# Optimization experiments

Hardware: AMD Instinct MI355X
Metric: run time of the kernel (lower is better)

## Reference

```python
import jax, jax.numpy as jnp
import numpy as np

WINDOW = 9
REG_WEIGHT = 1.0


def _box_filter(x, k):
    """Sum over a k^3 box via three separable 1D ones-convs (== conv3d with ones kernel)."""
    pad = k // 2
    for ax in range(3):  # D, H, W spatial axes
        kshape = [1, 1, 1, 1, 1]
        kshape[2 + ax] = k
        kern = jnp.ones(kshape, x.dtype)
        padding = [(pad, pad) if i == ax else (0, 0) for i in range(3)]
        x = jax.lax.conv_general_dilated(
            x, kern, window_strides=(1, 1, 1), padding=padding,
            dimension_numbers=("NCDHW", "OIDHW", "NCDHW"))
    return x


def _ncc_loss(pred, target, k):
    win_size = jnp.asarray(float(k ** 3), pred.dtype)
    pred_sum = _box_filter(pred, k)
    target_sum = _box_filter(target, k)
    pred_sq_sum = _box_filter(pred * pred, k)
    target_sq_sum = _box_filter(target * target, k)
    pred_target_sum = _box_filter(pred * target, k)
    pred_mean = pred_sum / win_size
    target_mean = target_sum / win_size
    cross = (pred_target_sum - target_mean * pred_sum - pred_mean * target_sum
             + pred_mean * target_mean * win_size)
    pred_var = pred_sq_sum - 2.0 * pred_mean * pred_sum + pred_mean * pred_mean * win_size
    target_var = target_sq_sum - 2.0 * target_mean * target_sum + target_mean * target_mean * win_size
    pred_var = jnp.clip(pred_var, 0.0, None)
    target_var = jnp.clip(target_var, 0.0, None)
    cc = cross * cross / (pred_var * target_var + 0.001)
    cc = jnp.clip(cc, 0.0, 1.0)
    return 1.0 - jnp.mean(cc)


def _gradient_loss(flow):
    dy = jnp.abs(flow[:, :, 1:, :, :] - flow[:, :, :-1, :, :])
    dx = jnp.abs(flow[:, :, :, 1:, :] - flow[:, :, :, :-1, :])
    dz = jnp.abs(flow[:, :, :, :, 1:] - flow[:, :, :, :, :-1])
    return (jnp.mean(dy) + jnp.mean(dx) + jnp.mean(dz)) / 3.0


def setup_inputs() -> dict:
    key = jax.random.key(0)
    k1, k2, k3 = jax.random.split(key, 3)
    B, D, H, W = 2, 160, 160, 160
    moved = jax.random.uniform(k1, (B, 1, D, H, W), dtype=jnp.float32)
    fixed = jax.random.uniform(k2, (B, 1, D, H, W), dtype=jnp.float32)
    flow = jax.random.normal(k3, (B, 3, D, H, W), dtype=jnp.float32)
    return {"moved": moved, "fixed": fixed, "flow": flow}


def reference(moved, fixed, flow):
    sim_loss = _ncc_loss(moved, fixed, WINDOW)
    reg_loss = _gradient_loss(flow)
    total_loss = sim_loss + REG_WEIGHT * reg_loss
    return total_loss
```

## Files before the change

### kernel.cpp

```cpp
#include <hip/hip_runtime.h>

#define DD 160
#define HH 160
#define WW 160
#define VOL (DD * HH * WW)
#define PLANE (HH * WW)
#define NB 2

#define CH 20
#define NDSP (DD / CH)
#define DSBLK (PLANE / 1024)
#define NDSUM (DSBLK * NDSP * NB)

#define GCHD 20
#define GBLK (NB * 3 * (DD / GCHD) * HH * (WW / 4) / 256)

#define HT 16
#define HS (HT + 8)
#define LDWH 168
#define WHBLK ((HH / HT) * DD * NB)

typedef _Float16 h8 __attribute__((ext_vector_type(8)));
typedef _Float16 h4 __attribute__((ext_vector_type(4)));

__global__ __launch_bounds__(256) void stream_pass(const float* __restrict__ mv,
                                                   const float* __restrict__ fx,
                                                   const float* __restrict__ fl,
                                                   _Float16* __restrict__ fields,
                                                   float* __restrict__ pg) {
    const int bx  = blockIdx.x;
    const int tid = threadIdx.x;

    if (bx < NDSUM) {
        const int qt  = bx % DSBLK;
        const int rem = bx / DSBLK;
        const int dsp = rem % NDSP;
        const int b   = rem / NDSP;
        const int hw  = (qt * 256 + tid) * 4;
        const int c0  = dsp * CH;
        const int cend = c0 + CH;

        const float* pm = mv + (size_t)b * VOL + hw;
        const float* pf = fx + (size_t)b * VOL + hw;
        _Float16*    fb = fields + (size_t)b * 5 * VOL + hw;

        float4 s0 = {0,0,0,0}, s1 = {0,0,0,0}, s2 = {0,0,0,0},
               s3 = {0,0,0,0}, s4 = {0,0,0,0};

#define ACC4(m4, f4, sgn)                                              \
        s0.x sgn m4.x; s0.y sgn m4.y; s0.z sgn m4.z; s0.w sgn m4.w;    \
        s1.x sgn f4.x; s1.y sgn f4.y; s1.z sgn f4.z; s1.w sgn f4.w;    \
        s2.x sgn m4.x * m4.x; s2.y sgn m4.y * m4.y;                    \
        s2.z sgn m4.z * m4.z; s2.w sgn m4.w * m4.w;                    \
        s3.x sgn f4.x * f4.x; s3.y sgn f4.y * f4.y;                    \
        s3.z sgn f4.z * f4.z; s3.w sgn f4.w * f4.w;                    \
        s4.x sgn m4.x * f4.x; s4.y sgn m4.y * f4.y;                    \
        s4.z sgn m4.z * f4.z; s4.w sgn m4.w * f4.w;

        {
            int lo = c0 - 4 > 0 ? c0 - 4 : 0;
            int hi = c0 + 4 < DD - 1 ? c0 + 4 : DD - 1;
            for (int dd = lo; dd <= hi; ++dd) {
                float4 m4 = *(const float4*)(pm + (size_t)dd * PLANE);
                float4 f4 = *(const float4*)(pf + (size_t)dd * PLANE);
                ACC4(m4, f4, +=)
            }
        }

        for (int d = c0; d < cend; ++d) {
            _Float16* o = fb + (size_t)d * PLANE;
            h4 t;
            t.x = (_Float16)s0.x; t.y = (_Float16)s0.y; t.z = (_Float16)s0.z; t.w = (_Float16)s0.w;
            *(h4*)(o + 0 * (size_t)VOL) = t;
            t.x = (_Float16)s1.x; t.y = (_Float16)s1.y; t.z = (_Float16)s1.z; t.w = (_Float16)s1.w;
            *(h4*)(o + 1 * (size_t)VOL) = t;
            t.x = (_Float16)s2.x; t.y = (_Float16)s2.y; t.z = (_Float16)s2.z; t.w = (_Float16)s2.w;
            *(h4*)(o + 2 * (size_t)VOL) = t;
            t.x = (_Float16)s3.x; t.y = (_Float16)s3.y; t.z = (_Float16)s3.z; t.w = (_Float16)s3.w;
            *(h4*)(o + 3 * (size_t)VOL) = t;
            t.x = (_Float16)s4.x; t.y = (_Float16)s4.y; t.z = (_Float16)s4.z; t.w = (_Float16)s4.w;
            *(h4*)(o + 4 * (size_t)VOL) = t;

            if (d + 1 < cend) {
                if (d + 5 < DD) {
                    float4 m4 = *(const float4*)(pm + (size_t)(d + 5) * PLANE);
                    float4 f4 = *(const float4*)(pf + (size_t)(d + 5) * PLANE);
                    ACC4(m4, f4, +=)
                }
                if (d - 4 >= 0) {
                    float4 m4 = *(const float4*)(pm + (size_t)(d - 4) * PLANE);
                    float4 f4 = *(const float4*)(pf + (size_t)(d - 4) * PLANE);
                    ACC4(m4, f4, -=)
                }
            }
        }
#undef ACC4
        return;
    }

    const int gid = (bx - NDSUM) * 256 + tid;
    const int w4  = gid % 40;
    int t = gid / 40;
    const int h  = t % HH;  t /= HH;
    const int dc = t % (DD / GCHD); t /= (DD / GCHD);
    const int bc = t;
    const int d0 = dc * GCHD;
    const int w  = w4 * 4;

    const float* base = fl + (size_t)bc * VOL;
    float acc = 0.f;
    float4 v = *(const float4*)(base + ((size_t)d0 * HH + h) * WW + w);
    for (int d = d0; d < d0 + GCHD; ++d) {
        const float* pd = base + ((size_t)d * HH + h) * WW + w;
        float4 vn = v;
        if (d < DD - 1) {
            vn = *(const float4*)(pd + PLANE);
            acc += fabsf(vn.x - v.x) + fabsf(vn.y - v.y) +
                   fabsf(vn.z - v.z) + fabsf(vn.w - v.w);
        }
        if (h < HH - 1) {
            float4 vh = *(const float4*)(pd + WW);
            acc += fabsf(vh.x - v.x) + fabsf(vh.y - v.y) +
                   fabsf(vh.z - v.z) + fabsf(vh.w - v.w);
        }
        acc += fabsf(v.y - v.x) + fabsf(v.z - v.y) + fabsf(v.w - v.z);
        if (w < WW - 4) acc += fabsf(pd[4] - v.w);
        v = vn;
    }

    for (int o = 32; o > 0; o >>= 1) acc += __shfl_down(acc, o, 64);
    __shared__ float red[4];
    int lane = tid & 63, wid = tid >> 6;
    if (lane == 0) red[wid] = acc;
    __syncthreads();
    if (tid == 0) pg[bx - NDSUM] = red[0] + red[1] + red[2] + red[3];
}

__global__ __launch_bounds__(512, 6) void ncc_whcc(const _Float16* __restrict__ fields,
                                                   float* __restrict__ partial) {
    __shared__ _Float16 ws[5][HS][LDWH];
    __shared__ float red[8];

    const int hx  = blockIdx.x;
    const int d   = blockIdx.y;
    const int b   = blockIdx.z;
    const int h0  = hx * HT;
    const int tid = threadIdx.x;

    if (tid < 480) {
        const int r  = tid / 20;
        const int s  = tid - r * 20;
        const int h  = h0 - 4 + r;
        const int w0 = 8 * s;
        const bool rowok = (unsigned)h < (unsigned)HH;

#pragma unroll
        for (int f = 0; f < 5; ++f) {
            float v[16];
#pragma unroll
            for (int i = 0; i < 16; ++i) v[i] = 0.f;
            if (rowok) {
                const _Float16* fr = fields + (size_t)(b * 5 + f) * VOL
                                            + ((size_t)d * HH + h) * WW;
                if (s > 0) {
                    h4 a = *(const h4*)(fr + w0 - 4);
                    v[0] = (float)a.x; v[1] = (float)a.y; v[2] = (float)a.z; v[3] = (float)a.w;
                }
                h4 a1 = *(const h4*)(fr + w0);
                v[4] = (float)a1.x; v[5] = (float)a1.y; v[6] = (float)a1.z; v[7] = (float)a1.w;
                h4 a2 = *(const h4*)(fr + w0 + 4);
                v[8] = (float)a2.x; v[9] = (float)a2.y; v[10] = (float)a2.z; v[11] = (float)a2.w;
                if (s < 19) {
                    h4 a3 = *(const h4*)(fr + w0 + 8);
                    v[12] = (float)a3.x; v[13] = (float)a3.y; v[14] = (float)a3.z; v[15] = (float)a3.w;
                }
            }
            float o[8];
            float sum = 0.f;
#pragma unroll
            for (int i = 0; i < 9; ++i) sum += v[i];
            o[0] = sum;
#pragma unroll
            for (int k = 1; k < 8; ++k) {
                sum += v[k + 8] - v[k - 1];
                o[k] = sum;
            }
            h8 pk;
#pragma unroll
            for (int j = 0; j < 8; ++j) pk[j] = (_Float16)o[j];
            *(h8*)&ws[f][r][w0] = pk;
        }
    }
    __syncthreads();

    float acc = 0.f;
    if (tid < 320) {
        const int ro  = tid / 20;
        const int oct = tid - ro * 20;
        const int w   = 8 * oct;

        float s0[8], s1[8], s2[8], s3[8], s4[8];
#pragma unroll
        for (int j = 0; j < 8; ++j) { s0[j]=0.f; s1[j]=0.f; s2[j]=0.f; s3[j]=0.f; s4[j]=0.f; }
#pragma unroll
        for (int t = 0; t < 9; ++t) {
            h8 v0 = *(const h8*)&ws[0][ro + t][w];
            h8 v1 = *(const h8*)&ws[1][ro + t][w];
            h8 v2 = *(const h8*)&ws[2][ro + t][w];
            h8 v3 = *(const h8*)&ws[3][ro + t][w];
            h8 v4 = *(const h8*)&ws[4][ro + t][w];
#pragma unroll
            for (int j = 0; j < 8; ++j) {
                s0[j] += (float)v0[j]; s1[j] += (float)v1[j];
                s2[j] += (float)v2[j]; s3[j] += (float)v3[j];
                s4[j] += (float)v4[j];
            }
        }
        const float inv_win = 1.0f / 729.0f;
#pragma unroll
        for (int j = 0; j < 8; ++j) {
            float cross = fmaf(-(s0[j] * s1[j]), inv_win, s4[j]);
            float pv = fmaxf(fmaf(-(s0[j] * s0[j]), inv_win, s2[j]), 0.f);
            float tv = fmaxf(fmaf(-(s1[j] * s1[j]), inv_win, s3[j]), 0.f);
            float cc = cross * cross / (pv * tv + 0.001f);
            acc += fminf(fmaxf(cc, 0.f), 1.f);
        }
    }

    for (int o = 32; o > 0; o >>= 1) acc += __shfl_down(acc, o, 64);
    int lane = tid & 63, wid = tid >> 6;
    if (lane == 0) red[wid] = acc;
    __syncthreads();
    if (tid == 0) {
        float r8 = 0.f;
#pragma unroll
        for (int i = 0; i < 8; ++i) r8 += red[i];
        partial[((size_t)b * DD + d) * (HH / HT) + hx] = r8;
    }
}

__global__ __launch_bounds__(256) void finalize(const float* __restrict__ pcc, int ncc,
                                                const float* __restrict__ pg, int ng,
                                                float* __restrict__ out) {
    __shared__ float red[4];
    int lane = threadIdx.x & 63, wid = threadIdx.x >> 6;

    float a = 0.f;
    for (int i = threadIdx.x; i < ncc; i += 256) a += pcc[i];
    for (int o = 32; o > 0; o >>= 1) a += __shfl_down(a, o, 64);
    if (lane == 0) red[wid] = a;
    __syncthreads();
    float asum = red[0] + red[1] + red[2] + red[3];
    __syncthreads();

    float g = 0.f;
    for (int i = threadIdx.x; i < ng; i += 256) g += pg[i];
    for (int o = 32; o > 0; o >>= 1) g += __shfl_down(g, o, 64);
    if (lane == 0) red[wid] = g;
    __syncthreads();
    float gsum = red[0] + red[1] + red[2] + red[3];

    if (threadIdx.x == 0) {
        float sim = 1.0f - asum / 8192000.0f;
        float reg = gsum / 73267200.0f;
        out[0] = sim + reg;
    }
}

extern "C" void kernel_launch(void* const* d_in, const int* in_sizes, int n_in,
                              void* d_out, int out_size, void* d_ws, size_t ws_size,
                              hipStream_t stream) {
    const float* moved  = (const float*)d_in[0];
    const float* fixedp = (const float*)d_in[1];
    const float* flow   = (const float*)d_in[2];
    float* out = (float*)d_out;

    _Float16* fields = (_Float16*)d_ws;
    float* pcc = (float*)(fields + (size_t)NB * 5 * VOL);
    float* pg  = pcc + WHBLK;

    stream_pass<<<NDSUM + GBLK, 256, 0, stream>>>(moved, fixedp, flow, fields, pg);
    ncc_whcc<<<dim3(HH / HT, DD, NB), 512, 0, stream>>>(fields, pcc);
    finalize<<<1, 256, 0, stream>>>(pcc, WHBLK, pg, GBLK, out);
}
```

Measured before the change: 115.4 us.

## Split gradient reduction into separate kernel and batch depth-sum stores in groups

The gradient-loss reduction moves out of the fused stream kernel into its own kernel, launched after the NCC kernel. The D-axis sliding-sum kernel now buffers five consecutive depth slices of all five fields in registers and issues their stores together, grouped by field. The aim is to give the store path more independent writes in flight and to cut branching in the depth-sum kernel. The cost is an extra kernel launch, and the gradient work no longer shares a grid with the depth-sum work, so it cannot fill idle compute units there.

```diff
diff --git a/kernel.cpp b/kernel.cpp
--- a/kernel.cpp
+++ b/kernel.cpp
@@ -7,79 +7,80 @@
 #define PLANE (HH * WW)
 #define NB 2
 
-#define CH 20
-#define NDSP (DD / CH)
+#define DCH 20
+#define NDSP (DD / DCH)
 #define DSBLK (PLANE / 1024)
 #define NDSUM (DSBLK * NDSP * NB)
-
-#define GCHD 20
-#define GBLK (NB * 3 * (DD / GCHD) * HH * (WW / 4) / 256)
+#define BG 5
 
 #define HT 16
 #define HS (HT + 8)
 #define LDWH 168
 #define WHBLK ((HH / HT) * DD * NB)
 
+#define GCHD 20
+#define GBLK (NB * 3 * (DD / GCHD) * HH * (WW / 4) / 256)
+
 typedef _Float16 h8 __attribute__((ext_vector_type(8)));
 typedef _Float16 h4 __attribute__((ext_vector_type(4)));
 
-__global__ __launch_bounds__(256) void stream_pass(const float* __restrict__ mv,
-                                                   const float* __restrict__ fx,
-                                                   const float* __restrict__ fl,
-                                                   _Float16* __restrict__ fields,
-                                                   float* __restrict__ pg) {
+__global__ __launch_bounds__(256) void dsum(const float* __restrict__ mv,
+                                            const float* __restrict__ fx,
+                                            _Float16* __restrict__ fields) {
     const int bx  = blockIdx.x;
     const int tid = threadIdx.x;
 
-    if (bx < NDSUM) {
-        const int qt  = bx % DSBLK;
-        const int rem = bx / DSBLK;
-        const int dsp = rem % NDSP;
-        const int b   = rem / NDSP;
-        const int hw  = (qt * 256 + tid) * 4;
-        const int c0  = dsp * CH;
-        const int cend = c0 + CH;
-
-        const float* pm = mv + (size_t)b * VOL + hw;
-        const float* pf = fx + (size_t)b * VOL + hw;
-        _Float16*    fb = fields + (size_t)b * 5 * VOL + hw;
-
-        float4 s0 = {0,0,0,0}, s1 = {0,0,0,0}, s2 = {0,0,0,0},
-               s3 = {0,0,0,0}, s4 = {0,0,0,0};
+    const int qt  = bx % DSBLK;
+    const int rem = bx / DSBLK;
+    const int dsp = rem % NDSP;
+    const int b   = rem / NDSP;
+    const int hw  = (qt * 256 + tid) * 4;
+    const int c0  = dsp * DCH;
+    const int cend = c0 + DCH;
+
+    const float* pm = mv + (size_t)b * VOL + hw;
+    const float* pf = fx + (size_t)b * VOL + hw;
+    _Float16*    fb = fields + (size_t)b * 5 * VOL + hw;
+
+    float4 s0 = {0,0,0,0}, s1 = {0,0,0,0}, s2 = {0,0,0,0},
+           s3 = {0,0,0,0}, s4 = {0,0,0,0};
 
 #define ACC4(m4, f4, sgn)                                              \
-        s0.x sgn m4.x; s0.y sgn m4.y; s0.z sgn m4.z; s0.w sgn m4.w;    \
-        s1.x sgn f4.x; s1.y sgn f4.y; s1.z sgn f4.z; s1.w sgn f4.w;    \
-        s2.x sgn m4.x * m4.x; s2.y sgn m4.y * m4.y;                    \
-        s2.z sgn m4.z * m4.z; s2.w sgn m4.w * m4.w;                    \
-        s3.x sgn f4.x * f4.x; s3.y sgn f4.y * f4.y;                    \
-        s3.z sgn f4.z * f4.z; s3.w sgn f4.w * f4.w;                    \
-        s4.x sgn m4.x * f4.x; s4.y sgn m4.y * f4.y;                    \
-        s4.z sgn m4.z * f4.z; s4.w sgn m4.w * f4.w;
-
-        {
-            int lo = c0 - 4 > 0 ? c0 - 4 : 0;
-            int hi = c0 + 4 < DD - 1 ? c0 + 4 : DD - 1;
-            for (int dd = lo; dd <= hi; ++dd) {
-                float4 m4 = *(const float4*)(pm + (size_t)dd * PLANE);
-                float4 f4 = *(const float4*)(pf + (size_t)dd * PLANE);
-                ACC4(m4, f4, +=)
-            }
-        }
-
-        for (int d = c0; d < cend; ++d) {
-            _Float16* o = fb + (size_t)d * PLANE;
-            h4 t;
-            t.x = (_Float16)s0.x; t.y = (_Float16)s0.y; t.z = (_Float16)s0.z; t.w = (_Float16)s0.w;
-            *(h4*)(o + 0 * (size_t)VOL) = t;
-            t.x = (_Float16)s1.x; t.y = (_Float16)s1.y; t.z = (_Float16)s1.z; t.w = (_Float16)s1.w;
-            *(h4*)(o + 1 * (size_t)VOL) = t;
-            t.x = (_Float16)s2.x; t.y = (_Float16)s2.y; t.z = (_Float16)s2.z; t.w = (_Float16)s2.w;
-            *(h4*)(o + 2 * (size_t)VOL) = t;
-            t.x = (_Float16)s3.x; t.y = (_Float16)s3.y; t.z = (_Float16)s3.z; t.w = (_Float16)s3.w;
-            *(h4*)(o + 3 * (size_t)VOL) = t;
-            t.x = (_Float16)s4.x; t.y = (_Float16)s4.y; t.z = (_Float16)s4.z; t.w = (_Float16)s4.w;
-            *(h4*)(o + 4 * (size_t)VOL) = t;
+    s0.x sgn m4.x; s0.y sgn m4.y; s0.z sgn m4.z; s0.w sgn m4.w;        \
+    s1.x sgn f4.x; s1.y sgn f4.y; s1.z sgn f4.z; s1.w sgn f4.w;        \
+    s2.x sgn m4.x * m4.x; s2.y sgn m4.y * m4.y;                        \
+    s2.z sgn m4.z * m4.z; s2.w sgn m4.w * m4.w;                        \
+    s3.x sgn f4.x * f4.x; s3.y sgn f4.y * f4.y;                        \
+    s3.z sgn f4.z * f4.z; s3.w sgn f4.w * f4.w;                        \
+    s4.x sgn m4.x * f4.x; s4.y sgn m4.y * f4.y;                        \
+    s4.z sgn m4.z * f4.z; s4.w sgn m4.w * f4.w;
+
+    {
+        int lo = c0 - 4 > 0 ? c0 - 4 : 0;
+        int hi = c0 + 4 < DD - 1 ? c0 + 4 : DD - 1;
+        for (int dd = lo; dd <= hi; ++dd) {
+            float4 m4 = *(const float4*)(pm + (size_t)dd * PLANE);
+            float4 f4 = *(const float4*)(pf + (size_t)dd * PLANE);
+            ACC4(m4, f4, +=)
+        }
+    }
+
+#pragma unroll
+    for (int g = 0; g < DCH / BG; ++g) {
+        h4 buf[BG][5];
+#pragma unroll
+        for (int k = 0; k < BG; ++k) {
+            const int d = c0 + g * BG + k;
+            buf[k][0].x = (_Float16)s0.x; buf[k][0].y = (_Float16)s0.y;
+            buf[k][0].z = (_Float16)s0.z; buf[k][0].w = (_Float16)s0.w;
+            buf[k][1].x = (_Float16)s1.x; buf[k][1].y = (_Float16)s1.y;
+            buf[k][1].z = (_Float16)s1.z; buf[k][1].w = (_Float16)s1.w;
+            buf[k][2].x = (_Float16)s2.x; buf[k][2].y = (_Float16)s2.y;
+            buf[k][2].z = (_Float16)s2.z; buf[k][2].w = (_Float16)s2.w;
+            buf[k][3].x = (_Float16)s3.x; buf[k][3].y = (_Float16)s3.y;
+            buf[k][3].z = (_Float16)s3.z; buf[k][3].w = (_Float16)s3.w;
+            buf[k][4].x = (_Float16)s4.x; buf[k][4].y = (_Float16)s4.y;
+            buf[k][4].z = (_Float16)s4.z; buf[k][4].w = (_Float16)s4.w;
 
             if (d + 1 < cend) {
                 if (d + 5 < DD) {
@@ -94,11 +95,124 @@
                 }
             }
         }
+#pragma unroll
+        for (int f = 0; f < 5; ++f) {
+#pragma unroll
+            for (int k = 0; k < BG; ++k) {
+                const int d = c0 + g * BG + k;
+                *(h4*)(fb + (size_t)f * VOL + (size_t)d * PLANE) = buf[k][f];
+            }
+        }
+    }
 #undef ACC4
-        return;
-    }
-
-    const int gid = (bx - NDSUM) * 256 + tid;
+}
+
+__global__ __launch_bounds__(512, 6) void ncc_whcc(const _Float16* __restrict__ fields,
+                                                   float* __restrict__ partial) {
+    __shared__ _Float16 ws[5][HS][LDWH];
+    __shared__ float red[8];
+
+    const int hx  = blockIdx.x;
+    const int d   = blockIdx.y;
+    const int b   = blockIdx.z;
+    const int h0  = hx * HT;
+    const int tid = threadIdx.x;
+
+    if (tid < 480) {
+        const int r  = tid / 20;
+        const int s  = tid - r * 20;
+        const int h  = h0 - 4 + r;
+        const int w0 = 8 * s;
+        const bool rowok = (unsigned)h < (unsigned)HH;
+
+#pragma unroll
+        for (int f = 0; f < 5; ++f) {
+            float v[16];
+#pragma unroll
+            for (int i = 0; i < 16; ++i) v[i] = 0.f;
+            if (rowok) {
+                const _Float16* fr = fields + (size_t)(b * 5 + f) * VOL
+                                            + ((size_t)d * HH + h) * WW;
+                if (s > 0) {
+                    h4 a = *(const h4*)(fr + w0 - 4);
+                    v[0] = (float)a.x; v[1] = (float)a.y; v[2] = (float)a.z; v[3] = (float)a.w;
+                }
+                h4 a1 = *(const h4*)(fr + w0);
+                v[4] = (float)a1.x; v[5] = (float)a1.y; v[6] = (float)a1.z; v[7] = (float)a1.w;
+                h4 a2 = *(const h4*)(fr + w0 + 4);
+                v[8] = (float)a2.x; v[9] = (float)a2.y; v[10] = (float)a2.z; v[11] = (float)a2.w;
+                if (s < 19) {
+                    h4 a3 = *(const h4*)(fr + w0 + 8);
+                    v[12] = (float)a3.x; v[13] = (float)a3.y; v[14] = (float)a3.z; v[15] = (float)a3.w;
+                }
+            }
+            float o[8];
+            float sum = 0.f;
+#pragma unroll
+            for (int i = 0; i < 9; ++i) sum += v[i];
+            o[0] = sum;
+#pragma unroll
+            for (int k = 1; k < 8; ++k) {
+                sum += v[k + 8] - v[k - 1];
+                o[k] = sum;
+            }
+            h8 pk;
+#pragma unroll
+            for (int j = 0; j < 8; ++j) pk[j] = (_Float16)o[j];
+            *(h8*)&ws[f][r][w0] = pk;
+        }
+    }
+    __syncthreads();
+
+    float acc = 0.f;
+    if (tid < 320) {
+        const int ro  = tid / 20;
+        const int oct = tid - ro * 20;
+        const int w   = 8 * oct;
+
+        float s0[8], s1[8], s2[8], s3[8], s4[8];
+#pragma unroll
+        for (int j = 0; j < 8; ++j) { s0[j]=0.f; s1[j]=0.f; s2[j]=0.f; s3[j]=0.f; s4[j]=0.f; }
+#pragma unroll
+        for (int t = 0; t < 9; ++t) {
+            h8 v0 = *(const h8*)&ws[0][ro + t][w];
+            h8 v1 = *(const h8*)&ws[1][ro + t][w];
+            h8 v2 = *(const h8*)&ws[2][ro + t][w];
+            h8 v3 = *(const h8*)&ws[3][ro + t][w];
+            h8 v4 = *(const h8*)&ws[4][ro + t][w];
+#pragma unroll
+            for (int j = 0; j < 8; ++j) {
+                s0[j] += (float)v0[j]; s1[j] += (float)v1[j];
+                s2[j] += (float)v2[j]; s3[j] += (float)v3[j];
+                s4[j] += (float)v4[j];
+            }
+        }
+        const float inv_win = 1.0f / 729.0f;
+#pragma unroll
+        for (int j = 0; j < 8; ++j) {
+            float cross = fmaf(-(s0[j] * s1[j]), inv_win, s4[j]);
+            float pv = fmaxf(fmaf(-(s0[j] * s0[j]), inv_win, s2[j]), 0.f);
+            float tv = fmaxf(fmaf(-(s1[j] * s1[j]), inv_win, s3[j]), 0.f);
+            float cc = cross * cross / (pv * tv + 0.001f);
+            acc += fminf(fmaxf(cc, 0.f), 1.f);
+        }
+    }
+
+    for (int o = 32; o > 0; o >>= 1) acc += __shfl_down(acc, o, 64);
+    int lane = tid & 63, wid = tid >> 6;
+    if (lane == 0) red[wid] = acc;
+    __syncthreads();
+    if (tid == 0) {
+        float r8 = 0.f;
+#pragma unroll
+        for (int i = 0; i < 8; ++i) r8 += red[i];
+        partial[((size_t)b * DD + d) * (HH / HT) + hx] = r8;
+    }
+}
+
+__global__ __launch_bounds__(256) void grad_red(const float* __restrict__ fl,
+                                                float* __restrict__ partial) {
+    const int gid = blockIdx.x * 256 + threadIdx.x;
     const int w4  = gid % 40;
     int t = gid / 40;
     const int h  = t % HH;  t /= HH;
@@ -130,113 +244,10 @@
 
     for (int o = 32; o > 0; o >>= 1) acc += __shfl_down(acc, o, 64);
     __shared__ float red[4];
-    int lane = tid & 63, wid = tid >> 6;
+    int lane = threadIdx.x & 63, wid = threadIdx.x >> 6;
     if (lane == 0) red[wid] = acc;
     __syncthreads();
-    if (tid == 0) pg[bx - NDSUM] = red[0] + red[1] + red[2] + red[3];
-}
-
-__global__ __launch_bounds__(512, 6) void ncc_whcc(const _Float16* __restrict__ fields,
-                                                   float* __restrict__ partial) {
-    __shared__ _Float16 ws[5][HS][LDWH];
-    __shared__ float red[8];
-
-    const int hx  = blockIdx.x;
-    const int d   = blockIdx.y;
-    const int b   = blockIdx.z;
-    const int h0  = hx * HT;
-    const int tid = threadIdx.x;
-
-    if (tid < 480) {
-        const int r  = tid / 20;
-        const int s  = tid - r * 20;
-        const int h  = h0 - 4 + r;
-        const int w0 = 8 * s;
-        const bool rowok = (unsigned)h < (unsigned)HH;
-
-#pragma unroll
-        for (int f = 0; f < 5; ++f) {
-            float v[16];
-#pragma unroll
-            for (int i = 0; i < 16; ++i) v[i] = 0.f;
-            if (rowok) {
-                const _Float16* fr = fields + (size_t)(b * 5 + f) * VOL
-                                            + ((size_t)d * HH + h) * WW;
-                if (s > 0) {
-                    h4 a = *(const h4*)(fr + w0 - 4);
-                    v[0] = (float)a.x; v[1] = (float)a.y; v[2] = (float)a.z; v[3] = (float)a.w;
-                }
-                h4 a1 = *(const h4*)(fr + w0);
-                v[4] = (float)a1.x; v[5] = (float)a1.y; v[6] = (float)a1.z; v[7] = (float)a1.w;
-                h4 a2 = *(const h4*)(fr + w0 + 4);
-                v[8] = (float)a2.x; v[9] = (float)a2.y; v[10] = (float)a2.z; v[11] = (float)a2.w;
-                if (s < 19) {
-                    h4 a3 = *(const h4*)(fr + w0 + 8);
-                    v[12] = (float)a3.x; v[13] = (float)a3.y; v[14] = (float)a3.z; v[15] = (float)a3.w;
-                }
-            }
-            float o[8];
-            float sum = 0.f;
-#pragma unroll
-            for (int i = 0; i < 9; ++i) sum += v[i];
-            o[0] = sum;
-#pragma unroll
-            for (int k = 1; k < 8; ++k) {
-                sum += v[k + 8] - v[k - 1];
-                o[k] = sum;
-            }
-            h8 pk;
-#pragma unroll
-            for (int j = 0; j < 8; ++j) pk[j] = (_Float16)o[j];
-            *(h8*)&ws[f][r][w0] = pk;
-        }
-    }
-    __syncthreads();
-
-    float acc = 0.f;
-    if (tid < 320) {
-        const int ro  = tid / 20;
-        const int oct = tid - ro * 20;
-        const int w   = 8 * oct;
-
-        float s0[8], s1[8], s2[8], s3[8], s4[8];
-#pragma unroll
-        for (int j = 0; j < 8; ++j) { s0[j]=0.f; s1[j]=0.f; s2[j]=0.f; s3[j]=0.f; s4[j]=0.f; }
-#pragma unroll
-        for (int t = 0; t < 9; ++t) {
-            h8 v0 = *(const h8*)&ws[0][ro + t][w];
-            h8 v1 = *(const h8*)&ws[1][ro + t][w];
-            h8 v2 = *(const h8*)&ws[2][ro + t][w];
-            h8 v3 = *(const h8*)&ws[3][ro + t][w];
-            h8 v4 = *(const h8*)&ws[4][ro + t][w];
-#pragma unroll
-            for (int j = 0; j < 8; ++j) {
-                s0[j] += (float)v0[j]; s1[j] += (float)v1[j];
-                s2[j] += (float)v2[j]; s3[j] += (float)v3[j];
-                s4[j] += (float)v4[j];
-            }
-        }
-        const float inv_win = 1.0f / 729.0f;
-#pragma unroll
-        for (int j = 0; j < 8; ++j) {
-            float cross = fmaf(-(s0[j] * s1[j]), inv_win, s4[j]);
-            float pv = fmaxf(fmaf(-(s0[j] * s0[j]), inv_win, s2[j]), 0.f);
-            float tv = fmaxf(fmaf(-(s1[j] * s1[j]), inv_win, s3[j]), 0.f);
-            float cc = cross * cross / (pv * tv + 0.001f);
-            acc += fminf(fmaxf(cc, 0.f), 1.f);
-        }
-    }
-
-    for (int o = 32; o > 0; o >>= 1) acc += __shfl_down(acc, o, 64);
-    int lane = tid & 63, wid = tid >> 6;
-    if (lane == 0) red[wid] = acc;
-    __syncthreads();
-    if (tid == 0) {
-        float r8 = 0.f;
-#pragma unroll
-        for (int i = 0; i < 8; ++i) r8 += red[i];
-        partial[((size_t)b * DD + d) * (HH / HT) + hx] = r8;
-    }
+    if (threadIdx.x == 0) partial[blockIdx.x] = red[0] + red[1] + red[2] + red[3];
 }
 
 __global__ __launch_bounds__(256) void finalize(const float* __restrict__ pcc, int ncc,
@@ -279,7 +290,8 @@
     float* pcc = (float*)(fields + (size_t)NB * 5 * VOL);
     float* pg  = pcc + WHBLK;
 
-    stream_pass<<<NDSUM + GBLK, 256, 0, stream>>>(moved, fixedp, flow, fields, pg);
+    dsum<<<NDSUM, 256, 0, stream>>>(moved, fixedp, fields);
     ncc_whcc<<<dim3(HH / HT, DD, NB), 512, 0, stream>>>(fields, pcc);
+    grad_red<<<GBLK, 256, 0, stream>>>(flow, pg);
     finalize<<<1, 256, 0, stream>>>(pcc, WHBLK, pg, GBLK, out);
 }
```

New measurement: 118.9 us. 3.0% more time.
